# Kernel optimization log

Measured on AMD Instinct MI355X. Metric: run time of the kernel, lower is better.

Reference implementation:

```python
import jax, jax.numpy as jnp
import numpy as np

NUM_HEADS = 16
EPS = 1e-6  # LinearAttention.epsilon

def setup_inputs() -> dict:
    key = jax.random.key(0)
    ks = jax.random.split(key, 10)
    B, L, D = 4, 4096, 2048
    s = 1.0 / np.sqrt(D)
    x = jax.random.normal(ks[0], (B, L, D), dtype=jnp.float32)
    attention_mask = jnp.ones((B, L), dtype=jnp.float32)
    Wq = jax.random.normal(ks[1], (D, D), dtype=jnp.float32) * s
    bq = jnp.zeros((D,), dtype=jnp.float32)
    Wk = jax.random.normal(ks[2], (D, D), dtype=jnp.float32) * s
    bk = jnp.zeros((D,), dtype=jnp.float32)
    Wv = jax.random.normal(ks[3], (D, D), dtype=jnp.float32) * s
    bv = jnp.zeros((D,), dtype=jnp.float32)
    Wo = jax.random.normal(ks[4], (D, D), dtype=jnp.float32) * s
    bo = jnp.zeros((D,), dtype=jnp.float32)
    return {"x": x, "attention_mask": attention_mask, "Wq": Wq, "bq": bq,
            "Wk": Wk, "bk": bk, "Wv": Wv, "bv": bv, "Wo": Wo, "bo": bo}

def reference(x, attention_mask, Wq, bq, Wk, bk, Wv, bv, Wo, bo):
    B, L, Dm = x.shape
    H = NUM_HEADS
    Dh = Dm // H
    # q/k/v projections -> [B, H, L, Dh]
    def proj(W, b):
        return (x @ W + b).reshape(B, L, H, Dh).transpose(0, 2, 1, 3)
    q = proj(Wq, bq)
    k = proj(Wk, bk)
    v = proj(Wv, bv)
    # feature map: elu(x) + 1
    q = jax.nn.elu(q) + 1.0
    k = jax.nn.elu(k) + 1.0
    # mask keys/values: mask [B, 1, L, 1]
    m = attention_mask[:, None, :, None]
    k = k * m
    v = v * m
    # causal linear attention via cumulative sums over sequence dim
    k_cum = jnp.cumsum(k, axis=2)          # [B,H,L,Dh]
    kv_cum = jnp.cumsum(k * v, axis=2)     # [B,H,L,Dh] (diagonal kv state, as in source)
    z = jnp.sum(q * k_cum, axis=-1) + EPS  # [B,H,L]
    z = z * attention_mask[:, None, :]
    out = (q * kv_cum) / z[..., None]      # [B,H,L,Dh]
    out = out.transpose(0, 2, 1, 3).reshape(B, L, Dm)
    return out @ Wo + bo
```

## Files before the change

### kernel.cpp

```cpp
#include <hip/hip_runtime.h>
#include <cstdint>
#include <cstddef>

#define EPS_F 1e-6f

__device__ inline unsigned short f2bf(float f) {
    union { float f; unsigned u; } v; v.f = f;
    unsigned r = v.u + 0x7fffu + ((v.u >> 16) & 1u);
    return (unsigned short)(r >> 16);
}
__device__ inline float bf2f(unsigned u16) {
    union { unsigned u; float f; } v; v.u = u16 << 16; return v.f;
}

typedef __attribute__((ext_vector_type(8))) __bf16 bf16x8;
typedef __attribute__((ext_vector_type(8))) short short8;
typedef __attribute__((ext_vector_type(8))) unsigned short ushort8;
typedef __attribute__((ext_vector_type(4))) float floatx4;

__device__ inline void async_load16(const void* g, void* l) {
    __builtin_amdgcn_global_load_lds((const __attribute__((address_space(1))) void*)g,
                                     (__attribute__((address_space(3))) void*)l,
                                     16, 0, 0);
}

__global__ void cast_x_kernel(const float* __restrict__ in, unsigned short* __restrict__ out, int n8) {
    int i = blockIdx.x * blockDim.x + threadIdx.x;
    if (i < n8) {
        float4 a = ((const float4*)in)[2 * i];
        float4 b = ((const float4*)in)[2 * i + 1];
        short8 o;
        o[0] = (short)f2bf(a.x); o[1] = (short)f2bf(a.y);
        o[2] = (short)f2bf(a.z); o[3] = (short)f2bf(a.w);
        o[4] = (short)f2bf(b.x); o[5] = (short)f2bf(b.y);
        o[6] = (short)f2bf(b.z); o[7] = (short)f2bf(b.w);
        ((short8*)out)[i] = o;
    }
}

__global__ void transpose_cast_kernel(const float* __restrict__ W0, const float* __restrict__ W1,
                                      const float* __restrict__ W2, const float* __restrict__ W3,
                                      unsigned short* __restrict__ WtBase, int n) {
    const float* W = (blockIdx.z == 0) ? W0 : (blockIdx.z == 1) ? W1 : (blockIdx.z == 2) ? W2 : W3;
    unsigned short* Wt = WtBase + (size_t)blockIdx.z * n * n;
    __shared__ float tile[32][33];
    int bx = blockIdx.x * 32;
    int by = blockIdx.y * 32;
    int tx = threadIdx.x;
    int ty = threadIdx.y;
    #pragma unroll
    for (int i = 0; i < 32; i += 8)
        tile[ty + i][tx] = W[(size_t)(by + ty + i) * n + bx + tx];
    __syncthreads();
    #pragma unroll
    for (int i = 0; i < 32; i += 8)
        Wt[(size_t)(bx + ty + i) * n + by + tx] = f2bf(tile[tx][ty + i]);
}

#define BMT 128
#define BNT 128
#define BKT 64
#define DMODEL 2048

template<int FINAL>
__global__ __launch_bounds__(256, 2)
void gemm_kernel(const unsigned short* __restrict__ A,
                 const unsigned short* __restrict__ Bt,
                 const float* __restrict__ b0, const float* __restrict__ b1,
                 const float* __restrict__ b2,
                 const float* __restrict__ mask,
                 unsigned short* __restrict__ qo, unsigned short* __restrict__ ko,
                 unsigned short* __restrict__ vo,
                 float* __restrict__ Cf,
                 int M, int K) {
    __shared__ __align__(16) unsigned short As[BMT * BKT];
    __shared__ __align__(16) unsigned short Bs[BNT * BKT];

    const int tid  = threadIdx.x;
    const int wave = tid >> 6;
    const int lane = tid & 63;
    const int m0    = blockIdx.x * BMT;
    const int nglob = blockIdx.y * BNT;
    int mat, n0;
    const float* bias;
    unsigned short* Cb = nullptr;
    if (FINAL) {
        mat = 0; n0 = nglob; bias = b0;
    } else {
        mat  = nglob >> 11;
        n0   = nglob & (DMODEL - 1);
        bias = (mat == 0) ? b0 : (mat == 1) ? b1 : b2;
        Cb   = (mat == 0) ? qo : (mat == 1) ? ko : vo;
    }
    const int wm = (wave >> 1) * 64;
    const int wn = (wave & 1) * 64;
    const int quad  = lane >> 4;
    const int row16 = lane & 15;

    floatx4 acc[4][4] = {};

    const int srow_lo = lane >> 3;
    const int schunk  = lane & 7;

    for (int k0 = 0; k0 < K; k0 += BKT) {
        #pragma unroll
        for (int i = 0; i < 4; i++) {
            int slot_base = wave * 256 + i * 64;
            int r  = wave * 32 + i * 8 + srow_lo;
            int cg = schunk ^ (r & 7);
            const unsigned short* ga = A  + (size_t)(m0 + r) * K + k0 + cg * 8;
            const unsigned short* gb = Bt + (size_t)(nglob + r) * K + k0 + cg * 8;
            async_load16(ga, As + (size_t)slot_base * 8);
            async_load16(gb, Bs + (size_t)slot_base * 8);
        }
        __syncthreads();

        #pragma unroll
        for (int kk = 0; kk < 2; kk++) {
            bf16x8 af[4], bfr[4];
            #pragma unroll
            for (int t = 0; t < 4; t++) {
                int ra = wm + t * 16 + row16;
                int ca = (kk * 4 + quad) ^ (ra & 7);
                af[t]  = __builtin_bit_cast(bf16x8, *(const short8*)(As + (size_t)ra * 64 + ca * 8));
                int rb = wn + t * 16 + row16;
                int cb = (kk * 4 + quad) ^ (rb & 7);
                bfr[t] = __builtin_bit_cast(bf16x8, *(const short8*)(Bs + (size_t)rb * 64 + cb * 8));
            }
            #pragma unroll
            for (int i = 0; i < 4; i++)
                #pragma unroll
                for (int j = 0; j < 4; j++)
                    acc[i][j] = __builtin_amdgcn_mfma_f32_16x16x32_bf16(af[i], bfr[j], acc[i][j], 0, 0, 0);
        }
        __syncthreads();
    }

    float bcache[4];
    #pragma unroll
    for (int j = 0; j < 4; j++) bcache[j] = bias[n0 + wn + j * 16 + row16];
    #pragma unroll
    for (int i = 0; i < 4; i++) {
        #pragma unroll
        for (int r = 0; r < 4; r++) {
            int row = m0 + wm + i * 16 + quad * 4 + r;
            float mr = 1.0f;
            if (!FINAL && mat >= 1) mr = mask[row];
            #pragma unroll
            for (int j = 0; j < 4; j++) {
                int col = n0 + wn + j * 16 + row16;
                float v = acc[i][j][r] + bcache[j];
                if (FINAL) {
                    Cf[(size_t)row * DMODEL + col] = v;
                } else {
                    if (mat <= 1) v = (v > 0.f) ? (v + 1.f) : __expf(v);
                    v *= mr;
                    Cb[(size_t)row * DMODEL + col] = f2bf(v);
                }
            }
        }
    }
}

#define SL    4096
#define SD    2048
#define SH    16
#define CHUNK 64
#define NCH   64

__global__ void scan_partial_kernel(const unsigned short* __restrict__ k,
                                    const unsigned short* __restrict__ v,
                                    float* __restrict__ sumK, float* __restrict__ sumKV) {
    int blk = blockIdx.x;
    int c = blk & (NCH - 1), bh = blk >> 6;
    int b = bh >> 4, h = bh & (SH - 1);
    int lane = threadIdx.x;
    int tg = lane >> 4, dg = lane & 15;
    size_t base = ((size_t)(b * SL + c * CHUNK + tg)) * SD + h * 128 + dg * 8;
    float sk[8] = {0.f, 0.f, 0.f, 0.f, 0.f, 0.f, 0.f, 0.f};
    float skv[8] = {0.f, 0.f, 0.f, 0.f, 0.f, 0.f, 0.f, 0.f};
    for (int it = 0; it < CHUNK / 4; it++) {
        ushort8 kw = *(const ushort8*)(k + base);
        ushort8 vw = *(const ushort8*)(v + base);
        #pragma unroll
        for (int j = 0; j < 8; j++) {
            float kf = bf2f(kw[j]);
            float vf = bf2f(vw[j]);
            sk[j] += kf; skv[j] += kf * vf;
        }
        base += (size_t)4 * SD;
    }
    #pragma unroll
    for (int j = 0; j < 8; j++) {
        sk[j]  += __shfl_xor(sk[j], 16);  sk[j]  += __shfl_xor(sk[j], 32);
        skv[j] += __shfl_xor(skv[j], 16); skv[j] += __shfl_xor(skv[j], 32);
    }
    if (tg == 0) {
        size_t o = ((size_t)bh * NCH + c) * 128 + dg * 8;
        *(float4*)(sumK  + o)     = make_float4(sk[0], sk[1], sk[2], sk[3]);
        *(float4*)(sumK  + o + 4) = make_float4(sk[4], sk[5], sk[6], sk[7]);
        *(float4*)(sumKV + o)     = make_float4(skv[0], skv[1], skv[2], skv[3]);
        *(float4*)(sumKV + o + 4) = make_float4(skv[4], skv[5], skv[6], skv[7]);
    }
}

__global__ void scan_offsets_kernel(const float* __restrict__ sumK, const float* __restrict__ sumKV,
                                    float* __restrict__ offK, float* __restrict__ offKV) {
    int bh = blockIdx.x;
    int d  = threadIdx.x;
    float aK = 0.f, aKV = 0.f;
    for (int c = 0; c < NCH; c++) {
        size_t o = ((size_t)bh * NCH + c) * 128 + d;
        float sk = sumK[o], skv = sumKV[o];
        offK[o] = aK; offKV[o] = aKV;
        aK += sk; aKV += skv;
    }
}

__global__ void scan_final_kernel(const unsigned short* __restrict__ q,
                                  const unsigned short* __restrict__ k,
                                  const unsigned short* __restrict__ v,
                                  const float* __restrict__ offK, const float* __restrict__ offKV,
                                  const float* __restrict__ mask,
                                  unsigned short* __restrict__ out) {
    int blk = blockIdx.x;
    int c = blk & (NCH - 1), bh = blk >> 6;
    int b = bh >> 4, h = bh & (SH - 1);
    int lane = threadIdx.x;
    size_t ob = ((size_t)bh * NCH + c) * 128 + 2 * lane;
    float2 kcv = *(const float2*)(offK  + ob);
    float2 kvv = *(const float2*)(offKV + ob);
    float kc0 = kcv.x, kc1 = kcv.y, kv0 = kvv.x, kv1 = kvv.y;
    size_t base = ((size_t)(b * SL + c * CHUNK)) * SD + h * 128 + 2 * lane;
    const float* mrow = mask + (size_t)b * SL + c * CHUNK;
    for (int s = 0; s < CHUNK / 4; s++) {
        unsigned kw[4], vw[4], qw[4];
        #pragma unroll
        for (int u = 0; u < 4; u++) {
            size_t a = base + (size_t)u * SD;
            kw[u] = *(const unsigned*)(k + a);
            vw[u] = *(const unsigned*)(v + a);
            qw[u] = *(const unsigned*)(q + a);
        }
        float p[4], n0[4], n1[4];
        #pragma unroll
        for (int u = 0; u < 4; u++) {
            float kk0 = bf2f(kw[u] & 0xffff), kk1 = bf2f(kw[u] >> 16);
            float vv0 = bf2f(vw[u] & 0xffff), vv1 = bf2f(vw[u] >> 16);
            float qq0 = bf2f(qw[u] & 0xffff), qq1 = bf2f(qw[u] >> 16);
            kc0 += kk0; kc1 += kk1;
            kv0 += kk0 * vv0; kv1 += kk1 * vv1;
            p[u]  = qq0 * kc0 + qq1 * kc1;
            n0[u] = qq0 * kv0; n1[u] = qq1 * kv1;
        }
        #pragma unroll
        for (int off = 32; off > 0; off >>= 1) {
            #pragma unroll
            for (int u = 0; u < 4; u++) p[u] += __shfl_xor(p[u], off);
        }
        #pragma unroll
        for (int u = 0; u < 4; u++) {
            float z = (p[u] + EPS_F) * mrow[s * 4 + u];
            float inv = 1.0f / z;
            unsigned o0 = f2bf(n0[u] * inv);
            unsigned o1 = f2bf(n1[u] * inv);
            *(unsigned*)(out + base + (size_t)u * SD) = o0 | (o1 << 16);
        }
        base += (size_t)4 * SD;
    }
}

extern "C" void kernel_launch(void* const* d_in, const int* in_sizes, int n_in,
                              void* d_out, int out_size, void* d_ws, size_t ws_size,
                              hipStream_t stream) {
    const float* x  = (const float*)d_in[0];
    const float* am = (const float*)d_in[1];
    const float* Wq = (const float*)d_in[2];
    const float* bq = (const float*)d_in[3];
    const float* Wk = (const float*)d_in[4];
    const float* bk = (const float*)d_in[5];
    const float* Wv = (const float*)d_in[6];
    const float* bv = (const float*)d_in[7];
    const float* Wo = (const float*)d_in[8];
    const float* bo = (const float*)d_in[9];
    float* out = (float*)d_out;

    const int Bb = 4, L = 4096, D = 2048;
    const int M = Bb * L;
    const size_t MD = (size_t)M * D;

    char* w = (char*)d_ws;
    unsigned short* xb    = (unsigned short*)w; w += MD * 2;
    unsigned short* qb    = (unsigned short*)w; w += MD * 2;
    unsigned short* kb    = (unsigned short*)w; w += MD * 2;
    unsigned short* vb    = (unsigned short*)w; w += MD * 2;
    unsigned short* WT    = (unsigned short*)w; w += (size_t)4 * D * D * 2;
    float* sumK  = (float*)w; w += (size_t)64 * NCH * 128 * 4;
    float* sumKV = (float*)w; w += (size_t)64 * NCH * 128 * 4;
    float* offK  = (float*)w; w += (size_t)64 * NCH * 128 * 4;
    float* offKV = (float*)w; w += (size_t)64 * NCH * 128 * 4;
    unsigned short* attnb = xb;

    int n8 = (int)(MD / 8);
    cast_x_kernel<<<(n8 + 255) / 256, 256, 0, stream>>>(x, xb, n8);
    dim3 tb(32, 8);
    dim3 tg(D / 32, D / 32, 4);
    transpose_cast_kernel<<<tg, tb, 0, stream>>>(Wq, Wk, Wv, Wo, WT, D);

    dim3 gq(M / BMT, 3 * D / BNT);
    gemm_kernel<0><<<gq, 256, 0, stream>>>(xb, WT, bq, bk, bv, am, qb, kb, vb, nullptr, M, D);

    scan_partial_kernel<<<64 * NCH, 64, 0, stream>>>(kb, vb, sumK, sumKV);
    scan_offsets_kernel<<<64, 128, 0, stream>>>(sumK, sumKV, offK, offKV);
    scan_final_kernel<<<64 * NCH, 64, 0, stream>>>(qb, kb, vb, offK, offKV, am, attnb);

    dim3 go(M / BMT, D / BNT);
    gemm_kernel<1><<<go, 256, 0, stream>>>(attnb, WT + (size_t)3 * D * D, bo, nullptr, nullptr,
                                           nullptr, nullptr, nullptr, nullptr, out, M, D);
}
```

Measured before the change: 915.8 us.

## Rewrite GEMM with 256x256 tiles, 4-stage async LDS pipeline and XCD swizzle

The bf16 MFMA GEMM goes from 128x128x64 tiles with a single buffer to 256x256x32 tiles with 512 threads. Global-to-LDS loads run through a 4-slot ring with prefetch depth 3, gated by explicit vmcnt waits and one barrier per step. It also adds a block-index swizzle across 8 XCDs, inline-asm ds_read_b128 and raised MFMA priority. The aim is to hide memory latency and raise reuse per tile, at the cost of more registers, 128KB of LDS that allows only one block per CU, and fragile hand-written waitcnt logic.

After: 911.6 us. No clear change (-0.5%).

```diff
diff --git a/kernel.cpp b/kernel.cpp
--- a/kernel.cpp
+++ b/kernel.cpp
@@ -17,12 +17,15 @@
 typedef __attribute__((ext_vector_type(8))) short short8;
 typedef __attribute__((ext_vector_type(8))) unsigned short ushort8;
 typedef __attribute__((ext_vector_type(4))) float floatx4;
+typedef __attribute__((ext_vector_type(4))) unsigned uintx4;
 
 __device__ inline void async_load16(const void* g, void* l) {
     __builtin_amdgcn_global_load_lds((const __attribute__((address_space(1))) void*)g,
                                      (__attribute__((address_space(3))) void*)l,
                                      16, 0, 0);
 }
+
+#define LDS_OFF(p) ((unsigned)(unsigned long long)(const __attribute__((address_space(3))) void*)(p))
 
 __global__ void cast_x_kernel(const float* __restrict__ in, unsigned short* __restrict__ out, int n8) {
     int i = blockIdx.x * blockDim.x + threadIdx.x;
@@ -57,13 +60,14 @@
         Wt[(size_t)(bx + ty + i) * n + by + tx] = f2bf(tile[tx][ty + i]);
 }
 
-#define BMT 128
-#define BNT 128
-#define BKT 64
+#define BMT 256
+#define BNT 256
+#define BKT 32
+#define SLOT_ELEMS (BMT * BKT)
 #define DMODEL 2048
 
 template<int FINAL>
-__global__ __launch_bounds__(256, 2)
+__global__ __launch_bounds__(512, 2)
 void gemm_kernel(const unsigned short* __restrict__ A,
                  const unsigned short* __restrict__ Bt,
                  const float* __restrict__ b0, const float* __restrict__ b1,
@@ -73,82 +77,113 @@
                  unsigned short* __restrict__ vo,
                  float* __restrict__ Cf,
                  int M, int K) {
-    __shared__ __align__(16) unsigned short As[BMT * BKT];
-    __shared__ __align__(16) unsigned short Bs[BNT * BKT];
+    __shared__ __align__(16) unsigned short As[4 * SLOT_ELEMS];
+    __shared__ __align__(16) unsigned short Bs[4 * SLOT_ELEMS];
 
     const int tid  = threadIdx.x;
+    const int lane = tid & 63;
     const int wave = tid >> 6;
-    const int lane = tid & 63;
-    const int m0    = blockIdx.x * BMT;
-    const int nglob = blockIdx.y * BNT;
-    int mat, n0;
-    const float* bias;
+    const int wr   = wave >> 2;
+    const int wc   = wave & 3;
+    const int quad  = lane >> 4;
+    const int row16 = lane & 15;
+
+    const int nwg = (int)(gridDim.x * gridDim.y);
+    const int bid = (int)(blockIdx.y * gridDim.x + blockIdx.x);
+    const int cpx = nwg >> 3;
+    const int swz = (bid & 7) * cpx + (bid >> 3);
+    const int bm  = swz % (int)gridDim.x;
+    const int bn  = swz / (int)gridDim.x;
+
+    const int m0    = bm * BMT;
+    const int nglob = bn * BNT;
+    int mat = 0, n0 = nglob;
+    const float* bias = b0;
     unsigned short* Cb = nullptr;
-    if (FINAL) {
-        mat = 0; n0 = nglob; bias = b0;
-    } else {
+    if (!FINAL) {
         mat  = nglob >> 11;
         n0   = nglob & (DMODEL - 1);
         bias = (mat == 0) ? b0 : (mat == 1) ? b1 : b2;
         Cb   = (mat == 0) ? qo : (mat == 1) ? ko : vo;
     }
-    const int wm = (wave >> 1) * 64;
-    const int wn = (wave & 1) * 64;
-    const int quad  = lane >> 4;
-    const int row16 = lane & 15;
-
-    floatx4 acc[4][4] = {};
-
-    const int srow_lo = lane >> 3;
-    const int schunk  = lane & 7;
-
-    for (int k0 = 0; k0 < K; k0 += BKT) {
-        #pragma unroll
-        for (int i = 0; i < 4; i++) {
-            int slot_base = wave * 256 + i * 64;
-            int r  = wave * 32 + i * 8 + srow_lo;
-            int cg = schunk ^ (r & 7);
-            const unsigned short* ga = A  + (size_t)(m0 + r) * K + k0 + cg * 8;
-            const unsigned short* gb = Bt + (size_t)(nglob + r) * K + k0 + cg * 8;
-            async_load16(ga, As + (size_t)slot_base * 8);
-            async_load16(gb, Bs + (size_t)slot_base * 8);
-        }
-        __syncthreads();
-
-        #pragma unroll
-        for (int kk = 0; kk < 2; kk++) {
-            bf16x8 af[4], bfr[4];
+
+    floatx4 acc[8][4] = {};
+
+    const unsigned short* gA[2];
+    const unsigned short* gB[2];
+    #pragma unroll
+    for (int b = 0; b < 2; b++) {
+        int s = b * 512 + tid;
+        int r = s >> 2, c = s & 3;
+        int cg = c ^ ((r >> 1) & 3);
+        gA[b] = A  + (size_t)(m0 + r) * K + cg * 8;
+        gB[b] = Bt + (size_t)(nglob + r) * K + cg * 8;
+    }
+
+    const unsigned asB = LDS_OFF(As);
+    const unsigned bsB = LDS_OFF(Bs);
+    const unsigned cP    = (unsigned)(quad ^ ((row16 >> 1) & 3));
+    const unsigned aLane = asB + (unsigned)(wr * 8192 + row16 * 64) + cP * 16u;
+    const unsigned bLane = bsB + (unsigned)(wc * 4096 + row16 * 64) + cP * 16u;
+
+    auto stage = [&](int tt, int sl) {
+        const int koff = tt * BKT;
+        #pragma unroll
+        for (int b = 0; b < 2; b++) {
+            int s = b * 512 + tid;
+            async_load16(gA[b] + koff, As + sl * SLOT_ELEMS + s * 8);
+            async_load16(gB[b] + koff, Bs + sl * SLOT_ELEMS + s * 8);
+        }
+    };
+
+    const int NT = K / BKT;
+    stage(0, 0); stage(1, 1); stage(2, 2);
+
+    for (int t = 0; t < NT; ++t) {
+        const int slot = t & 3;
+        if (t < NT - 2)       asm volatile("s_waitcnt vmcnt(8)" ::: "memory");
+        else if (t == NT - 2) asm volatile("s_waitcnt vmcnt(4)" ::: "memory");
+        else                  asm volatile("s_waitcnt vmcnt(0)" ::: "memory");
+        __builtin_amdgcn_s_barrier();
+        asm volatile("" ::: "memory");
+        if (t + 3 < NT) stage(t + 3, (t + 3) & 3);
+
+        const unsigned aOff = aLane + (unsigned)slot * (SLOT_ELEMS * 2);
+        const unsigned bOff = bLane + (unsigned)slot * (SLOT_ELEMS * 2);
+        uintx4 araw[8], braw[4];
+        #pragma unroll
+        for (int i = 0; i < 8; i++)
+            asm volatile("ds_read_b128 %0, %1" : "=v"(araw[i]) : "v"(aOff + (unsigned)(i * 1024)));
+        #pragma unroll
+        for (int j = 0; j < 4; j++)
+            asm volatile("ds_read_b128 %0, %1" : "=v"(braw[j]) : "v"(bOff + (unsigned)(j * 1024)));
+        asm volatile("s_waitcnt lgkmcnt(0)");
+        __builtin_amdgcn_sched_barrier(0);
+        __builtin_amdgcn_s_setprio(1);
+        #pragma unroll
+        for (int i = 0; i < 8; i++) {
+            bf16x8 af = __builtin_bit_cast(bf16x8, araw[i]);
             #pragma unroll
-            for (int t = 0; t < 4; t++) {
-                int ra = wm + t * 16 + row16;
-                int ca = (kk * 4 + quad) ^ (ra & 7);
-                af[t]  = __builtin_bit_cast(bf16x8, *(const short8*)(As + (size_t)ra * 64 + ca * 8));
-                int rb = wn + t * 16 + row16;
-                int cb = (kk * 4 + quad) ^ (rb & 7);
-                bfr[t] = __builtin_bit_cast(bf16x8, *(const short8*)(Bs + (size_t)rb * 64 + cb * 8));
-            }
-            #pragma unroll
-            for (int i = 0; i < 4; i++)
-                #pragma unroll
-                for (int j = 0; j < 4; j++)
-                    acc[i][j] = __builtin_amdgcn_mfma_f32_16x16x32_bf16(af[i], bfr[j], acc[i][j], 0, 0, 0);
-        }
-        __syncthreads();
+            for (int j = 0; j < 4; j++)
+                acc[i][j] = __builtin_amdgcn_mfma_f32_16x16x32_bf16(
+                    af, __builtin_bit_cast(bf16x8, braw[j]), acc[i][j], 0, 0, 0);
+        }
+        __builtin_amdgcn_s_setprio(0);
     }
 
     float bcache[4];
     #pragma unroll
-    for (int j = 0; j < 4; j++) bcache[j] = bias[n0 + wn + j * 16 + row16];
-    #pragma unroll
-    for (int i = 0; i < 4; i++) {
+    for (int j = 0; j < 4; j++) bcache[j] = bias[n0 + wc * 64 + j * 16 + row16];
+    #pragma unroll
+    for (int i = 0; i < 8; i++) {
         #pragma unroll
         for (int r = 0; r < 4; r++) {
-            int row = m0 + wm + i * 16 + quad * 4 + r;
+            int row = m0 + wr * 128 + i * 16 + quad * 4 + r;
             float mr = 1.0f;
             if (!FINAL && mat >= 1) mr = mask[row];
             #pragma unroll
             for (int j = 0; j < 4; j++) {
-                int col = n0 + wn + j * 16 + row16;
+                int col = n0 + wc * 64 + j * 16 + row16;
                 float v = acc[i][j][r] + bcache[j];
                 if (FINAL) {
                     Cf[(size_t)row * DMODEL + col] = v;
@@ -308,13 +343,13 @@
     transpose_cast_kernel<<<tg, tb, 0, stream>>>(Wq, Wk, Wv, Wo, WT, D);
 
     dim3 gq(M / BMT, 3 * D / BNT);
-    gemm_kernel<0><<<gq, 256, 0, stream>>>(xb, WT, bq, bk, bv, am, qb, kb, vb, nullptr, M, D);
+    gemm_kernel<0><<<gq, 512, 0, stream>>>(xb, WT, bq, bk, bv, am, qb, kb, vb, nullptr, M, D);
 
     scan_partial_kernel<<<64 * NCH, 64, 0, stream>>>(kb, vb, sumK, sumKV);
     scan_offsets_kernel<<<64, 128, 0, stream>>>(sumK, sumKV, offK, offKV);
     scan_final_kernel<<<64 * NCH, 64, 0, stream>>>(qb, kb, vb, offK, offKV, am, attnb);
 
     dim3 go(M / BMT, D / BNT);
-    gemm_kernel<1><<<go, 256, 0, stream>>>(attnb, WT + (size_t)3 * D * D, bo, nullptr, nullptr,
+    gemm_kernel<1><<<go, 512, 0, stream>>>(attnb, WT + (size_t)3 * D * D, bo, nullptr, nullptr,
                                            nullptr, nullptr, nullptr, nullptr, out, M, D);
 }
```
